# Performance work log

Hardware: AMD Instinct MI355X
Metric: run time of the kernel (lower is better)

The kernel has to match this reference:

```python
import jax, jax.numpy as jnp
import numpy as np

H_RES, W_RES = 32, 32
DIM = 512
NUM_HEADS = 16
HEAD_DIM = DIM // NUM_HEADS
SCALE = HEAD_DIM ** -0.5
B = 16
N = H_RES * W_RES
TABLE_SIZE = (2 * H_RES - 1) * (2 * W_RES - 1)


def _relative_position_index():
    coords_h = np.arange(H_RES)
    coords_w = np.arange(W_RES)
    coords = np.stack(np.meshgrid(coords_h, coords_w, indexing='ij'))  # [2, H, W]
    coords_flat = coords.reshape(2, -1)  # [2, N]
    rel = coords_flat[:, :, None] - coords_flat[:, None, :]  # [2, N, N]
    rel = rel.transpose(1, 2, 0).astype(np.int64)  # [N, N, 2]
    rel[:, :, 0] += H_RES - 1
    rel[:, :, 1] += W_RES - 1
    rel[:, :, 0] *= 2 * W_RES - 1
    return rel.sum(-1)  # [N, N]


def setup_inputs() -> dict:
    key = jax.random.key(0)
    ks = jax.random.split(key, 6)
    x = jax.random.normal(ks[0], (B, N, DIM), dtype=jnp.float32)
    w_qkv = jax.random.normal(ks[1], (DIM, 3 * DIM), dtype=jnp.float32) * (DIM ** -0.5)
    b_qkv = jnp.zeros((3 * DIM,), dtype=jnp.float32)
    w_proj = jax.random.normal(ks[2], (DIM, DIM), dtype=jnp.float32) * (DIM ** -0.5)
    b_proj = jnp.zeros((DIM,), dtype=jnp.float32)
    bias_table = jax.random.normal(ks[3], (TABLE_SIZE, NUM_HEADS), dtype=jnp.float32) * 0.02
    rel_index = jnp.asarray(_relative_position_index(), dtype=jnp.int32)
    return {"x": x, "w_qkv": w_qkv, "b_qkv": b_qkv, "w_proj": w_proj,
            "b_proj": b_proj, "bias_table": bias_table, "rel_index": rel_index}


def reference(x, w_qkv, b_qkv, w_proj, b_proj, bias_table, rel_index):
    Bq, Nq, C = x.shape
    qkv = x @ w_qkv + b_qkv  # [B, N, 3C]
    qkv = qkv.reshape(Bq, Nq, 3, NUM_HEADS, HEAD_DIM)
    q = qkv[:, :, 0].transpose(0, 2, 1, 3) * SCALE  # [B, nH, N, d]
    k = qkv[:, :, 1].transpose(0, 2, 1, 3)
    v = qkv[:, :, 2].transpose(0, 2, 1, 3)
    attn = jnp.einsum('bhnd,bhmd->bhnm', q, k)  # [B, nH, N, N]
    bias = bias_table[rel_index]  # [N, N, nH]
    attn = attn + bias.transpose(2, 0, 1)[None]  # broadcast over batch
    attn = jax.nn.softmax(attn, axis=-1)
    out = jnp.einsum('bhnm,bhmd->bhnd', attn, v)  # [B, nH, N, d]
    out = out.transpose(0, 2, 1, 3).reshape(Bq, Nq, C)
    return out @ w_proj + b_proj
```

## Files before the change

### kernel.cpp

```cpp
#include <hip/hip_runtime.h>
#include <hip/hip_bf16.h>
#include <cstdint>
#include <cstddef>

typedef _Float16 f16;
typedef __attribute__((ext_vector_type(8))) _Float16 f16x8;
typedef __attribute__((ext_vector_type(2))) _Float16 f16x2;
typedef __bf16 bf16;
typedef __attribute__((ext_vector_type(4))) float f32x4;
typedef __attribute__((ext_vector_type(16))) float f32x16;

#define LOG2E 1.4426950408889634f
#define QK_SCALE 0.17677669529663687f

__device__ __forceinline__ f32x4 mfma16f(f16x8 a, f16x8 b, f32x4 c) {
  return __builtin_amdgcn_mfma_f32_16x16x32_f16(a, b, c, 0, 0, 0);
}
__device__ __forceinline__ f32x16 mfma32f(f16x8 a, f16x8 b, f32x16 c) {
  return __builtin_amdgcn_mfma_f32_32x32x16_f16(a, b, c, 0, 0, 0);
}
__device__ __forceinline__ float exp2_hw(float x) {
  float r; asm("v_exp_f32 %0, %1" : "=v"(r) : "v"(x)); return r;
}
__device__ __forceinline__ uint32_t cvtpk_f16(float a, float b) {
  uint32_t r; asm("v_cvt_pkrtz_f16_f32 %0, %1, %2" : "=v"(r) : "v"(a), "v"(b)); return r;
}
__device__ __forceinline__ float lo16f(uint32_t u) { return __uint_as_float(u << 16); }
__device__ __forceinline__ float hi16raw(uint32_t u) { return __uint_as_float(u); }

__device__ __forceinline__ float dot2acc(uint32_t u, float acc) {
  union { uint32_t x; f16x2 h; } c; c.x = u;
  f16x2 one2 = {(_Float16)1.0f, (_Float16)1.0f};
  return __builtin_amdgcn_fdot2(c.h, one2, acc, false);
}

__device__ __forceinline__ void gl16(const f16* g, f16* l) {
  __builtin_amdgcn_global_load_lds(
      (const __attribute__((address_space(1))) void*)g,
      (__attribute__((address_space(3))) void*)l, 16, 0, 0);
}

__device__ __forceinline__ uint32_t packoff(int m, int k) {
  return (((uint32_t)(m >> 7) * 16u + (uint32_t)(k >> 5)) * 8u + (uint32_t)((m >> 4) & 7)) * 512u
       + (uint32_t)((k >> 3) & 3) * 128u + (uint32_t)(m & 15) * 8u + (uint32_t)(k & 7);
}

__global__ __launch_bounds__(256) void prep_kernel(
    const float* __restrict__ x, const float* __restrict__ wqkv, const float* __restrict__ wproj,
    f16* __restrict__ Xp, f16* __restrict__ Wq, f16* __restrict__ Wp)
{
  const int XT  = 16384 * 512 / 16;
  const int WQT = 1536 * 512 / 16;
  int t = blockIdx.x * 256 + threadIdx.x;
  if (t < XT) {
    uint32_t o = (uint32_t)t * 16u;
    uint32_t blk = o >> 9, rem = o & 511u;
    uint32_t k23 = rem >> 7, r16 = (rem >> 3) & 15u;
    uint32_t i7 = blk & 7u, k5 = (blk >> 3) & 15u, m7 = blk >> 7;
    uint32_t m = m7 * 128u + i7 * 16u + r16;
    uint32_t k = k5 * 32u + k23 * 8u;
    const float* s0 = x + (size_t)m * 512 + k;
    f32x4 a0 = *(const f32x4*)s0;
    f32x4 a1 = *(const f32x4*)(s0 + 4);
    f32x4 b0 = *(const f32x4*)(s0 + 512);
    f32x4 b1 = *(const f32x4*)(s0 + 516);
    f16 ov[16];
    #pragma unroll
    for (int j = 0; j < 4; ++j) {
      ov[j] = (f16)a0[j]; ov[4 + j] = (f16)a1[j];
      ov[8 + j] = (f16)b0[j]; ov[12 + j] = (f16)b1[j];
    }
    *(uint4*)(Xp + o) = *(uint4*)&ov[0];
    *(uint4*)(Xp + o + 8) = *(uint4*)&ov[8];
  } else if (t < XT + WQT) {
    uint32_t o = (uint32_t)(t - XT) * 16u;
    uint32_t blk = o >> 9, rem = o & 511u;
    uint32_t k23 = rem >> 7, r16 = (rem >> 3) & 15u;
    uint32_t i7 = blk & 7u, k5 = (blk >> 3) & 15u, m7 = blk >> 7;
    uint32_t n = m7 * 128u + i7 * 16u + r16;
    uint32_t k = k5 * 32u + k23 * 8u;
    f16 ov[16];
    #pragma unroll
    for (int j = 0; j < 8; ++j) {
      ov[j] = (f16)wqkv[(size_t)(k + j) * 1536 + n];
      ov[8 + j] = (f16)wqkv[(size_t)(k + j) * 1536 + n + 1];
    }
    *(uint4*)(Wq + o) = *(uint4*)&ov[0];
    *(uint4*)(Wq + o + 8) = *(uint4*)&ov[8];
  } else {
    uint32_t o = (uint32_t)(t - XT - WQT) * 16u;
    uint32_t blk = o >> 9, rem = o & 511u;
    uint32_t k23 = rem >> 7, r16 = (rem >> 3) & 15u;
    uint32_t i7 = blk & 7u, k5 = (blk >> 3) & 15u, m7 = blk >> 7;
    uint32_t n = m7 * 128u + i7 * 16u + r16;
    uint32_t k = k5 * 32u + k23 * 8u;
    f16 ov[16];
    #pragma unroll
    for (int j = 0; j < 8; ++j) {
      ov[j] = (f16)wproj[(size_t)(k + j) * 512 + n];
      ov[8 + j] = (f16)wproj[(size_t)(k + j) * 512 + n + 1];
    }
    *(uint4*)(Wp + o) = *(uint4*)&ov[0];
    *(uint4*)(Wp + o + 8) = *(uint4*)&ov[8];
  }
}

__global__ __launch_bounds__(256) void biasC_kernel(
    const float* __restrict__ btab, bf16* __restrict__ biasC)
{
  int t = blockIdx.x * 256 + threadIdx.x;
  if (t >= 16 * 63 * 64) return;
  int lane = t & 63;
  int sh = t >> 6;
  int s = sh % 63, h = sh / 63;
  int lq = lane & 31, hi5 = lane >> 5;
  int base = s * 63 + 31 + lq;
  bf16 o[16];
  #pragma unroll
  for (int r = 0; r < 16; ++r) {
    int kx = (r & 3) + 8 * (r >> 2) + 4 * hi5;
    o[r] = (bf16)(btab[(base - kx) * 16 + h] * LOG2E);
  }
  *(uint4*)(biasC + (size_t)t * 16) = *(uint4*)&o[0];
  *(uint4*)(biasC + (size_t)t * 16 + 8) = *(uint4*)&o[8];
}

template<int NB>
__global__ __launch_bounds__(256) void gemm_frag(
    const f16* __restrict__ Ap, const f16* __restrict__ Bp,
    const float* __restrict__ bvec,
    f16* __restrict__ Qp, f16* __restrict__ Kp, f16* __restrict__ Vt,
    float* __restrict__ out)
{
  __shared__ f16 sA[3][4096];
  __shared__ f16 sB[3][4096];
  const int bid = blockIdx.x;
  const int xcd = bid & 7, idx = bid >> 3;
  int mb, nb;
  if (NB == 12) { int q = idx / 12; mb = xcd * 16 + q; nb = idx - q * 12; }
  else          { mb = xcd * 16 + (idx >> 2); nb = idx & 3; }
  const int tid = threadIdx.x, lane = tid & 63, wave = tid >> 6;
  const int l15 = lane & 15, l4 = lane >> 4;
  const int wr = wave >> 1, wc = wave & 1;

  const f16* gA = Ap + (uint32_t)mb * 65536u + (uint32_t)wave * 1024u + (uint32_t)lane * 8u;
  const f16* gB = Bp + (uint32_t)nb * 65536u + (uint32_t)wave * 1024u + (uint32_t)lane * 8u;
  const int wl = wave * 1024;

  gl16(gA,        &sA[0][wl]);
  gl16(gA + 512,  &sA[0][wl + 512]);
  gl16(gB,        &sB[0][wl]);
  gl16(gB + 512,  &sB[0][wl + 512]);
  gl16(gA + 4096, &sA[1][wl]);
  gl16(gA + 4608, &sA[1][wl + 512]);
  gl16(gB + 4096, &sB[1][wl]);
  gl16(gB + 4608, &sB[1][wl + 512]);

  f32x4 acc[4][4];
  #pragma unroll
  for (int i = 0; i < 4; ++i)
    #pragma unroll
    for (int j = 0; j < 4; ++j) acc[i][j] = (f32x4){0.f, 0.f, 0.f, 0.f};

  const uint32_t aoff = (uint32_t)(wr * 4) * 512u + (uint32_t)lane * 8u;
  const uint32_t boff = (uint32_t)(wc * 4) * 512u + (uint32_t)lane * 8u;

  #pragma unroll
  for (int kt = 0; kt < 16; ++kt) {
    asm volatile("s_waitcnt vmcnt(4)" ::: "memory");
    asm volatile("s_barrier" ::: "memory");
    const int s2 = (kt + 2) % 3;
    gl16(gA + (kt + 2) * 4096,       &sA[s2][wl]);
    gl16(gA + (kt + 2) * 4096 + 512, &sA[s2][wl + 512]);
    gl16(gB + (kt + 2) * 4096,       &sB[s2][wl]);
    gl16(gB + (kt + 2) * 4096 + 512, &sB[s2][wl + 512]);
    __builtin_amdgcn_sched_barrier(0);
    const int s0 = kt % 3;
    f16x8 af[4], bfr[4];
    #pragma unroll
    for (int f = 0; f < 4; ++f) {
      af[f]  = *(const f16x8*)&sA[s0][aoff + f * 512];
      bfr[f] = *(const f16x8*)&sB[s0][boff + f * 512];
    }
    #pragma unroll
    for (int mf = 0; mf < 4; ++mf)
      #pragma unroll
      for (int nf = 0; nf < 4; ++nf)
        acc[mf][nf] = mfma16f(af[mf], bfr[nf], acc[mf][nf]);
  }
  asm volatile("s_waitcnt vmcnt(0)" ::: "memory");

  #pragma unroll
  for (int mf = 0; mf < 4; ++mf) {
    #pragma unroll
    for (int nf = 0; nf < 4; ++nf) {
      int colb = nb * 128 + wc * 64 + nf * 16 + l15;
      float bb = bvec[colb];
      #pragma unroll
      for (int i = 0; i < 4; ++i) {
        int m = mb * 128 + wr * 64 + mf * 16 + l4 * 4 + i;
        float v = acc[mf][nf][i] + bb;
        if (NB == 4) {
          out[(size_t)m * 512 + colb] = v;
        } else {
          int t = colb >> 9, cc = colb & 511;
          int b = m >> 10, n = m & 1023;
          int hh = cc >> 5, d = cc & 31;
          int bh2 = b * 16 + hh;
          if (t == 0) {
            v *= (QK_SCALE * LOG2E);
            uint32_t off = (((uint32_t)bh2 * 32u + (uint32_t)(n >> 5)) * 2u + (uint32_t)(d >> 4)) * 512u
                         + ((uint32_t)((d >> 3) & 1) * 32u + (uint32_t)(n & 31)) * 8u + (uint32_t)(d & 7);
            Qp[off] = (f16)v;
          } else if (t == 1) {
            Kp[((size_t)(bh2 * 2 + (d >> 4)) * 1024 + n) * 16 + (d & 15)] = (f16)v;
          } else {
            int nl = n & 15;
            int npl = (nl >= 4 && nl < 12) ? (nl ^ 12) : nl;
            int np = (n & ~15) | npl;
            Vt[((size_t)(bh2 * 128 + (np >> 3)) * 32 + d) * 8 + (np & 7)] = (f16)v;
          }
        }
      }
    }
  }
}

__global__ __launch_bounds__(256) void attn_kernel(
    const f16* __restrict__ Qp, const f16* __restrict__ Kp, const f16* __restrict__ Vt,
    const bf16* __restrict__ biasC, f16* __restrict__ Op)
{
  const int bid = blockIdx.x;
  const int xcd = bid & 7, slot = bid >> 3;
  const int h = xcd * 2 + (slot >> 6);
  const int rest = slot & 63;
  const int qg = rest >> 4, b = rest & 15;
  const int bh = b * 16 + h;
  const int tid = threadIdx.x, lane = tid & 63, wave = tid >> 6;
  const int lq = lane & 31, hi5 = lane >> 5;

  const int qb0 = qg * 8 + wave * 2;
  const int m0 = b * 1024 + qb0 * 32;

  const uint32_t qbase = ((uint32_t)bh * 32u + (uint32_t)qb0) * 1024u + (uint32_t)lane * 8u;
  const f16x8 q00 = *(const f16x8*)(Qp + qbase);
  const f16x8 q01 = *(const f16x8*)(Qp + qbase + 512);
  const f16x8 q10 = *(const f16x8*)(Qp + qbase + 1024);
  const f16x8 q11 = *(const f16x8*)(Qp + qbase + 1536);

  uint32_t koff = (uint32_t)bh * 32768u + (uint32_t)lq * 16u + (uint32_t)hi5 * 8u;
  uint32_t voff = (uint32_t)bh * 32768u + (uint32_t)hi5 * 256u + (uint32_t)lq * 8u;
  const bf16* bp = biasC + ((uint32_t)(h * 63 + qb0 + 31) * 64u + (uint32_t)lane) * 16u;

  f16x8 kA0 = *(const f16x8*)(Kp + koff);
  f16x8 kA1 = *(const f16x8*)(Kp + koff + 16384);
  uint4 p0A = *(const uint4*)(bp);
  uint4 p1A = *(const uint4*)(bp + 8);
  uint4 p2A = *(const uint4*)(bp + 1024);
  uint4 p3A = *(const uint4*)(bp + 1032);
  f16x8 vA0 = *(const f16x8*)(Vt + voff);
  f16x8 vA1 = *(const f16x8*)(Vt + voff + 512);
  f16x8 kB0 = *(const f16x8*)(Kp + koff + 512);
  f16x8 kB1 = *(const f16x8*)(Kp + koff + 16384 + 512);
  uint4 p0B = *(const uint4*)(bp - 1024);
  uint4 p1B = *(const uint4*)(bp - 1016);
  uint4 p2B = *(const uint4*)(bp);
  uint4 p3B = *(const uint4*)(bp + 8);
  f16x8 vB0 = *(const f16x8*)(Vt + voff + 1024);
  f16x8 vB1 = *(const f16x8*)(Vt + voff + 1536);

  f32x16 O0, O1;
  #pragma unroll
  for (int i = 0; i < 16; ++i) { O0[i] = 0.f; O1[i] = 0.f; }
  f32x4 racc0 = {0.f, 0.f, 0.f, 0.f}, racc1 = {0.f, 0.f, 0.f, 0.f};

  union Uf { uint32_t u[4]; f16x8 v; };

#define UNPACK16(S, Pa, Pb)                               \
  S[0]  = lo16f(Pa.x); S[1]  = hi16raw(Pa.x);             \
  S[2]  = lo16f(Pa.y); S[3]  = hi16raw(Pa.y);             \
  S[4]  = lo16f(Pa.z); S[5]  = hi16raw(Pa.z);             \
  S[6]  = lo16f(Pa.w); S[7]  = hi16raw(Pa.w);             \
  S[8]  = lo16f(Pb.x); S[9]  = hi16raw(Pb.x);             \
  S[10] = lo16f(Pb.y); S[11] = hi16raw(Pb.y);             \
  S[12] = lo16f(Pb.z); S[13] = hi16raw(Pb.z);             \
  S[14] = lo16f(Pb.w); S[15] = hi16raw(Pb.w);

  auto tile = [&](f16x8& K0, f16x8& K1, f16x8& V0, f16x8& V1,
                  uint4& P0, uint4& P1, uint4& P2, uint4& P3,
                  uint32_t kpre, uint32_t vpre, int bpre) {
    asm volatile("s_waitcnt vmcnt(8)" ::: "memory");
    f32x16 S0, S1;
    UNPACK16(S0, P0, P1)
    UNPACK16(S1, P2, P3)
    S0 = mfma32f(K0, q00, S0);
    S0 = mfma32f(K1, q01, S0);
    S1 = mfma32f(K0, q10, S1);
    S1 = mfma32f(K1, q11, S1);
    K0 = *(const f16x8*)(Kp + koff + kpre);
    K1 = *(const f16x8*)(Kp + koff + 16384 + kpre);
    P0 = *(const uint4*)(bp + bpre);
    P1 = *(const uint4*)(bp + bpre + 8);
    P2 = *(const uint4*)(bp + bpre + 1024);
    P3 = *(const uint4*)(bp + bpre + 1032);
    __builtin_amdgcn_sched_barrier(0);
    {
      float e0  = exp2_hw(S0[0]),  e1  = exp2_hw(S0[1]),  e2  = exp2_hw(S0[2]),  e3  = exp2_hw(S0[3]);
      float e4  = exp2_hw(S0[4]),  e5  = exp2_hw(S0[5]),  e6  = exp2_hw(S0[6]),  e7  = exp2_hw(S0[7]);
      float e8  = exp2_hw(S0[8]),  e9  = exp2_hw(S0[9]),  e10 = exp2_hw(S0[10]), e11 = exp2_hw(S0[11]);
      float e12 = exp2_hw(S0[12]), e13 = exp2_hw(S0[13]), e14 = exp2_hw(S0[14]), e15 = exp2_hw(S0[15]);
      Uf a1, a2;
      a1.u[0] = cvtpk_f16(e0,  e1);  a1.u[1] = cvtpk_f16(e2,  e3);
      a1.u[2] = cvtpk_f16(e4,  e5);  a1.u[3] = cvtpk_f16(e6,  e7);
      a2.u[0] = cvtpk_f16(e8,  e9);  a2.u[1] = cvtpk_f16(e10, e11);
      a2.u[2] = cvtpk_f16(e12, e13); a2.u[3] = cvtpk_f16(e14, e15);
      racc0[0] = dot2acc(a1.u[0], racc0[0]); racc0[1] = dot2acc(a1.u[1], racc0[1]);
      racc0[2] = dot2acc(a1.u[2], racc0[2]); racc0[3] = dot2acc(a1.u[3], racc0[3]);
      racc0[0] = dot2acc(a2.u[0], racc0[0]); racc0[1] = dot2acc(a2.u[1], racc0[1]);
      racc0[2] = dot2acc(a2.u[2], racc0[2]); racc0[3] = dot2acc(a2.u[3], racc0[3]);
      O0 = mfma32f(a1.v, V0, O0);
      O0 = mfma32f(a2.v, V1, O0);
    }
    {
      float e0  = exp2_hw(S1[0]),  e1  = exp2_hw(S1[1]),  e2  = exp2_hw(S1[2]),  e3  = exp2_hw(S1[3]);
      float e4  = exp2_hw(S1[4]),  e5  = exp2_hw(S1[5]),  e6  = exp2_hw(S1[6]),  e7  = exp2_hw(S1[7]);
      float e8  = exp2_hw(S1[8]),  e9  = exp2_hw(S1[9]),  e10 = exp2_hw(S1[10]), e11 = exp2_hw(S1[11]);
      float e12 = exp2_hw(S1[12]), e13 = exp2_hw(S1[13]), e14 = exp2_hw(S1[14]), e15 = exp2_hw(S1[15]);
      Uf a1, a2;
      a1.u[0] = cvtpk_f16(e0,  e1);  a1.u[1] = cvtpk_f16(e2,  e3);
      a1.u[2] = cvtpk_f16(e4,  e5);  a1.u[3] = cvtpk_f16(e6,  e7);
      a2.u[0] = cvtpk_f16(e8,  e9);  a2.u[1] = cvtpk_f16(e10, e11);
      a2.u[2] = cvtpk_f16(e12, e13); a2.u[3] = cvtpk_f16(e14, e15);
      racc1[0] = dot2acc(a1.u[0], racc1[0]); racc1[1] = dot2acc(a1.u[1], racc1[1]);
      racc1[2] = dot2acc(a1.u[2], racc1[2]); racc1[3] = dot2acc(a1.u[3], racc1[3]);
      racc1[0] = dot2acc(a2.u[0], racc1[0]); racc1[1] = dot2acc(a2.u[1], racc1[1]);
      racc1[2] = dot2acc(a2.u[2], racc1[2]); racc1[3] = dot2acc(a2.u[3], racc1[3]);
      O1 = mfma32f(a1.v, V0, O1);
      O1 = mfma32f(a2.v, V1, O1);
    }
    V0 = *(const f16x8*)(Vt + voff + vpre);
    V1 = *(const f16x8*)(Vt + voff + vpre + 512);
    __builtin_amdgcn_sched_barrier(0);
  };

  #pragma unroll 1
  for (int it = 0; it < 16; ++it) {
    tile(kA0, kA1, vA0, vA1, p0A, p1A, p2A, p3A, 1024u, 2048u, -2048);
    tile(kB0, kB1, vB0, vB1, p0B, p1B, p2B, p3B, 1536u, 3072u, -3072);
    koff += 1024u; voff += 2048u; bp -= 2048;
  }

  float rs0 = (racc0[0] + racc0[1]) + (racc0[2] + racc0[3]);
  rs0 += __shfl_xor(rs0, 32);
  float inv0 = 1.0f / rs0;
  float rs1 = (racc1[0] + racc1[1]) + (racc1[2] + racc1[3]);
  rs1 += __shfl_xor(rs1, 32);
  float inv1 = 1.0f / rs1;

  const int kcol = h * 32 + lq;
  #pragma unroll
  for (int r = 0; r < 16; ++r) {
    int qrow = (r & 3) + 8 * (r >> 2) + 4 * hi5;
    float t0 = __shfl(inv0, qrow);
    float t1 = __shfl(inv1, qrow);
    Op[packoff(m0 + qrow, kcol)] = (f16)(O0[r] * t0);
    Op[packoff(m0 + 32 + qrow, kcol)] = (f16)(O1[r] * t1);
  }
}

extern "C" void kernel_launch(void* const* d_in, const int* in_sizes, int n_in,
                              void* d_out, int out_size, void* d_ws, size_t ws_size,
                              hipStream_t stream) {
  const float* x     = (const float*)d_in[0];
  const float* wqkv  = (const float*)d_in[1];
  const float* bqkv  = (const float*)d_in[2];
  const float* wproj = (const float*)d_in[3];
  const float* bproj = (const float*)d_in[4];
  const float* btab  = (const float*)d_in[5];
  float* out = (float*)d_out;

  char* ws = (char*)d_ws;
  size_t off = 0;
  auto walloc = [&](size_t bytes) {
    void* p = ws + off;
    off += (bytes + 255) & ~(size_t)255;
    return p;
  };
  const size_t PAD = 262144;
  f16* Xp   = (f16*)walloc((size_t)16384 * 512 * 2 + PAD);
  f16* Wq   = (f16*)walloc((size_t)1536 * 512 * 2 + PAD);
  f16* Wp   = (f16*)walloc((size_t)512 * 512 * 2 + PAD);
  f16* Qp   = (f16*)walloc((size_t)16384 * 512 * 2 + PAD);
  f16* Kp   = (f16*)walloc((size_t)16384 * 512 * 2 + PAD);
  f16* Vt   = (f16*)walloc((size_t)16384 * 512 * 2 + PAD);
  bf16* biasC = (bf16*)walloc((size_t)16 * 63 * 64 * 16 * 2 + PAD);
  f16* Op   = (f16*)walloc((size_t)16384 * 512 * 2 + PAD);

  const int prep_blocks = (16384 * 512 / 16 + 1536 * 512 / 16 + 512 * 512 / 16) / 256;
  prep_kernel<<<prep_blocks, 256, 0, stream>>>(x, wqkv, wproj, Xp, Wq, Wp);

  biasC_kernel<<<(16 * 63 * 64 + 255) / 256, 256, 0, stream>>>(btab, biasC);

  gemm_frag<12><<<1536, 256, 0, stream>>>(
      Xp, Wq, bqkv, Qp, Kp, Vt, nullptr);

  attn_kernel<<<1024, 256, 0, stream>>>(Qp, Kp, Vt, biasC, Op);

  gemm_frag<4><<<512, 256, 0, stream>>>(
      Op, Wp, bproj, nullptr, nullptr, nullptr, out);
}
```

Measured before the change: 150.5 us.

## Split attention KV range across wave pairs and fuse bias prep into prep kernel

Each attention block now assigns two waves per query-block pair, each processing half of the key/value sequence, and combines partial outputs and row sums through shared memory before normalizing. The grid doubles to 2048 blocks, which shortens each wave's serial loop and raises parallelism, at the cost of LDS traffic, a block barrier, and idle combine-side waves. Separately, the bias-table reformatting kernel is folded into the prep kernel to remove one launch.

```diff
diff --git a/kernel.cpp b/kernel.cpp
--- a/kernel.cpp
+++ b/kernel.cpp
@@ -47,10 +47,13 @@
 
 __global__ __launch_bounds__(256) void prep_kernel(
     const float* __restrict__ x, const float* __restrict__ wqkv, const float* __restrict__ wproj,
-    f16* __restrict__ Xp, f16* __restrict__ Wq, f16* __restrict__ Wp)
+    const float* __restrict__ btab,
+    f16* __restrict__ Xp, f16* __restrict__ Wq, f16* __restrict__ Wp,
+    bf16* __restrict__ biasC)
 {
   const int XT  = 16384 * 512 / 16;
   const int WQT = 1536 * 512 / 16;
+  const int WPT = 512 * 512 / 16;
   int t = blockIdx.x * 256 + threadIdx.x;
   if (t < XT) {
     uint32_t o = (uint32_t)t * 16u;
@@ -87,7 +90,7 @@
     }
     *(uint4*)(Wq + o) = *(uint4*)&ov[0];
     *(uint4*)(Wq + o + 8) = *(uint4*)&ov[8];
-  } else {
+  } else if (t < XT + WQT + WPT) {
     uint32_t o = (uint32_t)(t - XT - WQT) * 16u;
     uint32_t blk = o >> 9, rem = o & 511u;
     uint32_t k23 = rem >> 7, r16 = (rem >> 3) & 15u;
@@ -102,27 +105,24 @@
     }
     *(uint4*)(Wp + o) = *(uint4*)&ov[0];
     *(uint4*)(Wp + o + 8) = *(uint4*)&ov[8];
-  }
-}
-
-__global__ __launch_bounds__(256) void biasC_kernel(
-    const float* __restrict__ btab, bf16* __restrict__ biasC)
-{
-  int t = blockIdx.x * 256 + threadIdx.x;
-  if (t >= 16 * 63 * 64) return;
-  int lane = t & 63;
-  int sh = t >> 6;
-  int s = sh % 63, h = sh / 63;
-  int lq = lane & 31, hi5 = lane >> 5;
-  int base = s * 63 + 31 + lq;
-  bf16 o[16];
-  #pragma unroll
-  for (int r = 0; r < 16; ++r) {
-    int kx = (r & 3) + 8 * (r >> 2) + 4 * hi5;
-    o[r] = (bf16)(btab[(base - kx) * 16 + h] * LOG2E);
-  }
-  *(uint4*)(biasC + (size_t)t * 16) = *(uint4*)&o[0];
-  *(uint4*)(biasC + (size_t)t * 16 + 8) = *(uint4*)&o[8];
+  } else {
+    int t2 = t - (XT + WQT + WPT);
+    if (t2 < 16 * 63 * 64) {
+      int lane = t2 & 63;
+      int sh = t2 >> 6;
+      int s = sh % 63, h = sh / 63;
+      int lq = lane & 31, hi5 = lane >> 5;
+      int base = s * 63 + 31 + lq;
+      bf16 o[16];
+      #pragma unroll
+      for (int r = 0; r < 16; ++r) {
+        int kx = (r & 3) + 8 * (r >> 2) + 4 * hi5;
+        o[r] = (bf16)(btab[(base - kx) * 16 + h] * LOG2E);
+      }
+      *(uint4*)(biasC + (size_t)t2 * 16) = *(uint4*)&o[0];
+      *(uint4*)(biasC + (size_t)t2 * 16 + 8) = *(uint4*)&o[8];
+    }
+  }
 }
 
 template<int NB>
@@ -230,16 +230,20 @@
     const f16* __restrict__ Qp, const f16* __restrict__ Kp, const f16* __restrict__ Vt,
     const bf16* __restrict__ biasC, f16* __restrict__ Op)
 {
+  __shared__ float combO[2][32][64];
+  __shared__ float combR[2][2][64];
+
   const int bid = blockIdx.x;
   const int xcd = bid & 7, slot = bid >> 3;
-  const int h = xcd * 2 + (slot >> 6);
-  const int rest = slot & 63;
-  const int qg = rest >> 4, b = rest & 15;
+  const int h = xcd * 2 + (slot >> 7);
+  const int rest = slot & 127;
+  const int qq = rest >> 4, b = rest & 15;
   const int bh = b * 16 + h;
   const int tid = threadIdx.x, lane = tid & 63, wave = tid >> 6;
   const int lq = lane & 31, hi5 = lane >> 5;
-
-  const int qb0 = qg * 8 + wave * 2;
+  const int pair = wave >> 1, kvh = wave & 1;
+
+  const int qb0 = qq * 4 + pair * 2;
   const int m0 = b * 1024 + qb0 * 32;
 
   const uint32_t qbase = ((uint32_t)bh * 32u + (uint32_t)qb0) * 1024u + (uint32_t)lane * 8u;
@@ -248,9 +252,9 @@
   const f16x8 q10 = *(const f16x8*)(Qp + qbase + 1024);
   const f16x8 q11 = *(const f16x8*)(Qp + qbase + 1536);
 
-  uint32_t koff = (uint32_t)bh * 32768u + (uint32_t)lq * 16u + (uint32_t)hi5 * 8u;
-  uint32_t voff = (uint32_t)bh * 32768u + (uint32_t)hi5 * 256u + (uint32_t)lq * 8u;
-  const bf16* bp = biasC + ((uint32_t)(h * 63 + qb0 + 31) * 64u + (uint32_t)lane) * 16u;
+  uint32_t koff = (uint32_t)bh * 32768u + (uint32_t)lq * 16u + (uint32_t)hi5 * 8u + (uint32_t)kvh * 8192u;
+  uint32_t voff = (uint32_t)bh * 32768u + (uint32_t)hi5 * 256u + (uint32_t)lq * 8u + (uint32_t)kvh * 16384u;
+  const bf16* bp = biasC + ((uint32_t)(h * 63 + qb0 + 31 - kvh * 16) * 64u + (uint32_t)lane) * 16u;
 
   f16x8 kA0 = *(const f16x8*)(Kp + koff);
   f16x8 kA1 = *(const f16x8*)(Kp + koff + 16384);
@@ -344,27 +348,48 @@
   };
 
   #pragma unroll 1
-  for (int it = 0; it < 16; ++it) {
+  for (int it = 0; it < 8; ++it) {
     tile(kA0, kA1, vA0, vA1, p0A, p1A, p2A, p3A, 1024u, 2048u, -2048);
     tile(kB0, kB1, vB0, vB1, p0B, p1B, p2B, p3B, 1536u, 3072u, -3072);
     koff += 1024u; voff += 2048u; bp -= 2048;
   }
 
-  float rs0 = (racc0[0] + racc0[1]) + (racc0[2] + racc0[3]);
-  rs0 += __shfl_xor(rs0, 32);
-  float inv0 = 1.0f / rs0;
-  float rs1 = (racc1[0] + racc1[1]) + (racc1[2] + racc1[3]);
-  rs1 += __shfl_xor(rs1, 32);
-  float inv1 = 1.0f / rs1;
-
-  const int kcol = h * 32 + lq;
-  #pragma unroll
-  for (int r = 0; r < 16; ++r) {
-    int qrow = (r & 3) + 8 * (r >> 2) + 4 * hi5;
-    float t0 = __shfl(inv0, qrow);
-    float t1 = __shfl(inv1, qrow);
-    Op[packoff(m0 + qrow, kcol)] = (f16)(O0[r] * t0);
-    Op[packoff(m0 + 32 + qrow, kcol)] = (f16)(O1[r] * t1);
+  float rsA = (racc0[0] + racc0[1]) + (racc0[2] + racc0[3]);
+  float rsB = (racc1[0] + racc1[1]) + (racc1[2] + racc1[3]);
+
+  if (kvh == 1) {
+    #pragma unroll
+    for (int r = 0; r < 16; ++r) {
+      combO[pair][r][lane] = O0[r];
+      combO[pair][16 + r][lane] = O1[r];
+    }
+    combR[pair][0][lane] = rsA;
+    combR[pair][1][lane] = rsB;
+  }
+  __syncthreads();
+  if (kvh == 0) {
+    #pragma unroll
+    for (int r = 0; r < 16; ++r) {
+      O0[r] += combO[pair][r][lane];
+      O1[r] += combO[pair][16 + r][lane];
+    }
+    rsA += combR[pair][0][lane];
+    rsB += combR[pair][1][lane];
+
+    float rs0 = rsA + __shfl_xor(rsA, 32);
+    float inv0 = 1.0f / rs0;
+    float rs1 = rsB + __shfl_xor(rsB, 32);
+    float inv1 = 1.0f / rs1;
+
+    const int kcol = h * 32 + lq;
+    #pragma unroll
+    for (int r = 0; r < 16; ++r) {
+      int qrow = (r & 3) + 8 * (r >> 2) + 4 * hi5;
+      float t0 = __shfl(inv0, qrow);
+      float t1 = __shfl(inv1, qrow);
+      Op[packoff(m0 + qrow, kcol)] = (f16)(O0[r] * t0);
+      Op[packoff(m0 + 32 + qrow, kcol)] = (f16)(O1[r] * t1);
+    }
   }
 }
 
@@ -396,15 +421,14 @@
   bf16* biasC = (bf16*)walloc((size_t)16 * 63 * 64 * 16 * 2 + PAD);
   f16* Op   = (f16*)walloc((size_t)16384 * 512 * 2 + PAD);
 
-  const int prep_blocks = (16384 * 512 / 16 + 1536 * 512 / 16 + 512 * 512 / 16) / 256;
-  prep_kernel<<<prep_blocks, 256, 0, stream>>>(x, wqkv, wproj, Xp, Wq, Wp);
-
-  biasC_kernel<<<(16 * 63 * 64 + 255) / 256, 256, 0, stream>>>(btab, biasC);
+  const int prep_total = 16384 * 512 / 16 + 1536 * 512 / 16 + 512 * 512 / 16 + 16 * 63 * 64;
+  prep_kernel<<<(prep_total + 255) / 256, 256, 0, stream>>>(
+      x, wqkv, wproj, btab, Xp, Wq, Wp, biasC);
 
   gemm_frag<12><<<1536, 256, 0, stream>>>(
       Xp, Wq, bqkv, Qp, Kp, Vt, nullptr);
 
-  attn_kernel<<<1024, 256, 0, stream>>>(Qp, Kp, Vt, biasC, Op);
+  attn_kernel<<<2048, 256, 0, stream>>>(Qp, Kp, Vt, biasC, Op);
 
   gemm_frag<4><<<512, 256, 0, stream>>>(
       Op, Wp, bproj, nullptr, nullptr, nullptr, out);
```

Result: no change. 153.3 us (+1.9%).
